# Performance work log

Hardware: AMD Instinct MI355X
Metric: run time of the kernel (lower is better)

The kernel has to match this reference:

```python
import jax, jax.numpy as jnp
import numpy as np

B, S, E, H = 2, 2048, 1024, 16
D = E // H  # head dimension = 64


def setup_inputs() -> dict:
    key = jax.random.key(0)
    ks = jax.random.split(key, 12)
    scale_in = 1.0 / np.sqrt(E)
    x = jax.random.normal(ks[0], (B, S, E), dtype=jnp.float32)
    # random 0/1 attention mask (1 = attend, 0 = masked out)
    mask = jax.random.randint(ks[1], (B, S, S), 0, 2, dtype=jnp.int32)
    # per-head QKV projections, stacked over the head axis: [H, E, D]
    Wq = jax.random.normal(ks[2], (H, E, D), dtype=jnp.float32) * scale_in
    bq = jnp.zeros((H, D), dtype=jnp.float32)
    Wk = jax.random.normal(ks[3], (H, E, D), dtype=jnp.float32) * scale_in
    bk = jnp.zeros((H, D), dtype=jnp.float32)
    Wv = jax.random.normal(ks[4], (H, E, D), dtype=jnp.float32) * scale_in
    bv = jnp.zeros((H, D), dtype=jnp.float32)
    # output projection: [H*D, E] == [E, E]
    Wo = jax.random.normal(ks[5], (H * D, E), dtype=jnp.float32) * scale_in
    bo = jnp.zeros((E,), dtype=jnp.float32)
    return {"x": x, "mask": mask, "Wq": Wq, "bq": bq, "Wk": Wk, "bk": bk,
            "Wv": Wv, "bv": bv, "Wo": Wo, "bo": bo}


def reference(x, mask, Wq, bq, Wk, bk, Wv, bv, Wo, bo):
    # Batched equivalent of the per-head Python loop: all heads at once.
    q = jnp.einsum('bse,hed->bhsd', x, Wq) + bq[None, :, None, :]  # [B,H,S,D]
    k = jnp.einsum('bse,hed->bhsd', x, Wk) + bk[None, :, None, :]
    v = jnp.einsum('bse,hed->bhsd', x, Wv) + bv[None, :, None, :]
    scale = 1.0 / jnp.sqrt(jnp.asarray(D, dtype=q.dtype))
    scores = jnp.einsum('bhsd,bhtd->bhst', q, k) * scale          # [B,H,S,S]
    scores = jnp.where(mask[:, None, :, :] != 0, scores, jnp.asarray(-1e9, scores.dtype))
    attn = jax.nn.softmax(scores, axis=-1)
    ctx = jnp.einsum('bhst,bhtd->bhsd', attn, v)                  # [B,H,S,D]
    # concat heads along feature dim (torch.cat(dim=2))
    concat = jnp.transpose(ctx, (0, 2, 1, 3)).reshape(B, S, H * D)
    return concat @ Wo + bo
```

## Files before the change

### kernel.cpp

```cpp
#include <hip/hip_runtime.h>

#define S_LEN 2048
#define EMB   1024
#define NH    16
#define HD    64
#define BS    2
#define QSCALE 0.18033688f

typedef __bf16 bf16;
typedef bf16  bf16x8 __attribute__((ext_vector_type(8)));
typedef bf16  bf16x4 __attribute__((ext_vector_type(4)));
typedef float f32x4  __attribute__((ext_vector_type(4)));
typedef unsigned long long u64;
typedef unsigned int u32;

__device__ __forceinline__ bf16x8 ld8(const bf16* p){ return *(const bf16x8*)p; }

__device__ __forceinline__ void gl_lds16(const bf16* g, void* l) {
    __builtin_amdgcn_global_load_lds(
        (const __attribute__((address_space(1))) void*)g,
        (__attribute__((address_space(3))) void*)l,
        16, 0, 0);
}

#define SW(row, g) ((((g) ^ ((row) & 7))) * 8)

__global__ __launch_bounds__(256)
void pack_mask(const int* __restrict__ mask, u64* __restrict__ pm)
{
    int lane = threadIdx.x & 63;
    int row  = blockIdx.x * 4 + (threadIdx.x >> 6);
    const int* mr = mask + (size_t)row * S_LEN;
    u64* pr = pm + (size_t)row * (S_LEN / 64);
    for (int i = 0; i < S_LEN / 64; ++i) {
        u64 bits = __ballot(mr[i * 64 + lane] != 0);
        if (lane == 0) pr[i] = bits;
    }
}

__global__ __launch_bounds__(256)
void transpose_w(const float* __restrict__ W0, const float* __restrict__ W1,
                 const float* __restrict__ W2, const float* __restrict__ W3,
                 bf16* __restrict__ Wt)
{
    const int z = blockIdx.z;
    const float* W = z == 0 ? W0 : z == 1 ? W1 : z == 2 ? W2 : W3;
    const bool head = z < 3;
    const int k0 = blockIdx.x * 64, n0 = blockIdx.y * 64;
    const int tid = threadIdx.x;
    __shared__ float T[64][68];
    {
        int k = k0 + (tid >> 2), cg = (tid & 3) * 16;
        size_t base = head ? ((size_t)(n0 >> 6) * ((size_t)EMB * HD) + (size_t)k * HD + cg)
                           : ((size_t)k * EMB + n0 + cg);
        #pragma unroll
        for (int g = 0; g < 4; ++g) {
            f32x4 v = *(const f32x4*)(W + base + g * 4);
            #pragma unroll
            for (int j = 0; j < 4; ++j) T[tid >> 2][cg + g * 4 + j] = v[j];
        }
    }
    __syncthreads();
    {
        int n = n0 + (tid >> 2), ck = (tid & 3) * 16;
        bf16 t16[16];
        #pragma unroll
        for (int j = 0; j < 16; ++j) t16[j] = (bf16)T[ck + j][tid >> 2];
        bf16* outp = Wt + (size_t)z * EMB * EMB + (size_t)n * EMB + k0 + ck;
        *(bf16x8*)outp       = *(bf16x8*)t16;
        *(bf16x8*)(outp + 8) = *(bf16x8*)(t16 + 8);
    }
}

__global__ __launch_bounds__(256)
void cvt_f32_bf16(const float* __restrict__ x, bf16* __restrict__ y)
{
    size_t i = ((size_t)blockIdx.x * 256 + threadIdx.x) * 16;
    bf16 t[16];
    #pragma unroll
    for (int g = 0; g < 4; ++g) {
        f32x4 v = *(const f32x4*)(x + i + g * 4);
        #pragma unroll
        for (int j = 0; j < 4; ++j) t[g * 4 + j] = (bf16)v[j];
    }
    *(bf16x8*)(y + i)     = *(bf16x8*)t;
    *(bf16x8*)(y + i + 8) = *(bf16x8*)(t + 8);
}

__global__ __launch_bounds__(256)
void scale_q(bf16* __restrict__ q)
{
    size_t i = ((size_t)blockIdx.x * 256 + threadIdx.x) * 8;
    bf16x8 v = *(bf16x8*)(q + i);
    #pragma unroll
    for (int j = 0; j < 8; ++j) v[j] = (bf16)((float)v[j] * QSCALE);
    *(bf16x8*)(q + i) = v;
}

__global__ __launch_bounds__(256)
void gemm_qkv(const void* __restrict__ Ap, const bf16* __restrict__ Wt,
              const float* __restrict__ bqp, const float* __restrict__ bkp,
              const float* __restrict__ bvp,
              bf16* __restrict__ qb, bf16* __restrict__ kb, bf16* __restrict__ VT,
              int a32)
{
    const int tid  = threadIdx.x;
    const int lane = tid & 63, quad = lane >> 4, c = lane & 15;
    const int w = tid >> 6, wm = w >> 1, wn = w & 1;
    const int m0 = blockIdx.x * 128;
    const int n0 = blockIdx.y * 128;

    __shared__ bf16 Ash[128][64];
    __shared__ bf16 Wsh[128][64];

    f32x4 acc[4][4];
    #pragma unroll
    for (int mt = 0; mt < 4; ++mt)
        #pragma unroll
        for (int nt = 0; nt < 4; ++nt) acc[mt][nt] = (f32x4){0.f,0.f,0.f,0.f};

    const int lrow = lane >> 3, lcol = (lane & 7) * 8;

    for (int k0 = 0; k0 < EMB; k0 += 64) {
        __syncthreads();
        if (!a32) {
            const bf16* A = (const bf16*)Ap;
            #pragma unroll
            for (int j = 0; j < 4; ++j)
                gl_lds16(A + (size_t)(m0 + w * 32 + j * 8 + lrow) * EMB + k0 + lcol,
                         &Ash[w * 32 + j * 8][0]);
        } else {
            const float* A = (const float*)Ap + (size_t)(m0 + (tid >> 1)) * EMB + k0 + (tid & 1) * 32;
            bf16 t[32];
            #pragma unroll
            for (int g = 0; g < 8; ++g) {
                f32x4 v = *(const f32x4*)(A + g * 4);
                #pragma unroll
                for (int j = 0; j < 4; ++j) t[g * 4 + j] = (bf16)v[j];
            }
            #pragma unroll
            for (int g2 = 0; g2 < 4; ++g2)
                *(bf16x8*)&Ash[tid >> 1][(tid & 1) * 32 + g2 * 8] = *(bf16x8*)(t + g2 * 8);
        }
        #pragma unroll
        for (int j = 0; j < 4; ++j)
            gl_lds16(Wt + (size_t)(n0 + w * 32 + j * 8 + lrow) * EMB + k0 + lcol,
                     &Wsh[w * 32 + j * 8][0]);
        __syncthreads();

        #pragma unroll
        for (int kh = 0; kh < 2; ++kh) {
            bf16x8 af[4], bfv[4];
            #pragma unroll
            for (int mt = 0; mt < 4; ++mt) af[mt]  = ld8(&Ash[wm * 64 + mt * 16 + c][kh * 32 + quad * 8]);
            #pragma unroll
            for (int nt = 0; nt < 4; ++nt) bfv[nt] = ld8(&Wsh[wn * 64 + nt * 16 + c][kh * 32 + quad * 8]);
            #pragma unroll
            for (int mt = 0; mt < 4; ++mt)
                #pragma unroll
                for (int nt = 0; nt < 4; ++nt)
                    acc[mt][nt] = __builtin_amdgcn_mfma_f32_16x16x32_bf16(af[mt], bfv[nt], acc[mt][nt], 0, 0, 0);
        }
    }

    const int z = n0 >> 10;
    const float* bias = z == 0 ? bqp : z == 1 ? bkp : bvp;
    #pragma unroll
    for (int nt = 0; nt < 4; ++nt) {
        int nn = (n0 & 1023) + wn * 64 + nt * 16 + c;
        float bv_ = bias[nn];
        #pragma unroll
        for (int mt = 0; mt < 4; ++mt)
            #pragma unroll
            for (int r = 0; r < 4; ++r) {
                int m = m0 + wm * 64 + mt * 16 + quad * 4 + r;
                float v = acc[mt][nt][r] + bv_;
                if (z == 0)      qb[(size_t)m * EMB + nn] = (bf16)(v * QSCALE);
                else if (z == 1) kb[(size_t)m * EMB + nn] = (bf16)v;
                else {
                    int head = nn >> 6, d = nn & 63;
                    VT[((size_t)((m >> 11) * NH + head) * HD + d) * S_LEN + (m & 2047)] = (bf16)v;
                }
            }
    }
}

__global__ __launch_bounds__(256)
void gemm_o(const bf16* __restrict__ Ap, const bf16* __restrict__ Wt,
            const float* __restrict__ bo, float* __restrict__ C)
{
    const int tid  = threadIdx.x;
    const int lane = tid & 63, quad = lane >> 4, c = lane & 15;
    const int w = tid >> 6, wm = w >> 1, wn = w & 1;
    const int m0 = blockIdx.x * 128;
    const int n0 = blockIdx.y * 64;

    __shared__ bf16 Ash[128][64];
    __shared__ bf16 Wsh[64][64];

    f32x4 acc[4][2];
    #pragma unroll
    for (int mt = 0; mt < 4; ++mt)
        #pragma unroll
        for (int nt = 0; nt < 2; ++nt) acc[mt][nt] = (f32x4){0.f,0.f,0.f,0.f};

    const int lrow = lane >> 3, lcol = (lane & 7) * 8;

    for (int k0 = 0; k0 < EMB; k0 += 64) {
        __syncthreads();
        #pragma unroll
        for (int j = 0; j < 4; ++j)
            gl_lds16(Ap + (size_t)(m0 + w * 32 + j * 8 + lrow) * EMB + k0 + lcol,
                     &Ash[w * 32 + j * 8][0]);
        #pragma unroll
        for (int j = 0; j < 2; ++j)
            gl_lds16(Wt + (size_t)(n0 + w * 16 + j * 8 + lrow) * EMB + k0 + lcol,
                     &Wsh[w * 16 + j * 8][0]);
        __syncthreads();

        #pragma unroll
        for (int kh = 0; kh < 2; ++kh) {
            bf16x8 af[4], bfv[2];
            #pragma unroll
            for (int mt = 0; mt < 4; ++mt) af[mt]  = ld8(&Ash[wm * 64 + mt * 16 + c][kh * 32 + quad * 8]);
            #pragma unroll
            for (int nt = 0; nt < 2; ++nt) bfv[nt] = ld8(&Wsh[wn * 32 + nt * 16 + c][kh * 32 + quad * 8]);
            #pragma unroll
            for (int mt = 0; mt < 4; ++mt)
                #pragma unroll
                for (int nt = 0; nt < 2; ++nt)
                    acc[mt][nt] = __builtin_amdgcn_mfma_f32_16x16x32_bf16(af[mt], bfv[nt], acc[mt][nt], 0, 0, 0);
        }
    }

    #pragma unroll
    for (int nt = 0; nt < 2; ++nt) {
        int n = n0 + wn * 32 + nt * 16 + c;
        float bv_ = bo[n];
        #pragma unroll
        for (int mt = 0; mt < 4; ++mt)
            #pragma unroll
            for (int r = 0; r < 4; ++r) {
                int m = m0 + wm * 64 + mt * 16 + quad * 4 + r;
                C[(size_t)m * EMB + n] = acc[mt][nt][r] + bv_;
            }
    }
}

__global__ __launch_bounds__(512)
void gemm128(const void* __restrict__ Ap, const float* __restrict__ Wp,
             const bf16* __restrict__ Wtp, const float* __restrict__ bias,
             void* __restrict__ Cp, int N, int K, int whead,
             int m_base, int a32, int cmode)
{
    const int tid  = threadIdx.x;
    const int lane = tid & 63, quad = lane >> 4, c = lane & 15;
    const int w = tid >> 6, wm = w >> 2, wn = w & 3;
    const int m0 = blockIdx.x * 128, n0 = blockIdx.y * 128;

    __shared__ bf16 Ash[128][64];
    __shared__ bf16 Wsh[128][64];

    f32x4 acc[4][2];
    #pragma unroll
    for (int mt = 0; mt < 4; ++mt)
        #pragma unroll
        for (int nt = 0; nt < 2; ++nt) acc[mt][nt] = (f32x4){0.f,0.f,0.f,0.f};

    const int arow = tid >> 2, aq = tid & 3;

    auto compute = [&]() {
        #pragma unroll
        for (int kh = 0; kh < 2; ++kh) {
            bf16x8 bfr[2];
            #pragma unroll
            for (int nt = 0; nt < 2; ++nt) {
                int rw = wn * 32 + nt * 16 + c;
                bfr[nt] = ld8(&Wsh[rw][SW(rw, kh * 4 + quad)]);
            }
            #pragma unroll
            for (int mt = 0; mt < 4; ++mt) {
                int ra = wm * 64 + mt * 16 + c;
                bf16x8 af = ld8(&Ash[ra][SW(ra, kh * 4 + quad)]);
                #pragma unroll
                for (int nt = 0; nt < 2; ++nt)
                    acc[mt][nt] = __builtin_amdgcn_mfma_f32_16x16x32_bf16(af, bfr[nt], acc[mt][nt], 0, 0, 0);
            }
        }
    };

    for (int k0 = 0; k0 < K; k0 += 64) {
        __syncthreads();
        if (a32) {
            const float* A = (const float*)Ap + (size_t)(m_base + m0 + arow) * K + k0 + aq * 16;
            bf16 t16[16];
            #pragma unroll
            for (int g = 0; g < 4; ++g) {
                f32x4 v = *(const f32x4*)(A + g * 4);
                #pragma unroll
                for (int j = 0; j < 4; ++j) t16[g * 4 + j] = (bf16)v[j];
            }
            *(bf16x8*)&Ash[arow][SW(arow, aq * 2)]     = *(bf16x8*)t16;
            *(bf16x8*)&Ash[arow][SW(arow, aq * 2 + 1)] = *(bf16x8*)(t16 + 8);
        } else {
            const bf16* A = (const bf16*)Ap + (size_t)(m_base + m0 + arow) * K + k0 + aq * 16;
            *(bf16x8*)&Ash[arow][SW(arow, aq * 2)]     = ld8(A);
            *(bf16x8*)&Ash[arow][SW(arow, aq * 2 + 1)] = ld8(A + 8);
        }
        {
            int nl = tid & 127, kg = tid >> 7;
            int n = n0 + nl;
            size_t base    = whead ? ((size_t)(n >> 6) * ((size_t)K * HD) + (n & 63))
                                   : (size_t)n;
            size_t kstride = whead ? (size_t)HD : (size_t)N;
            #pragma unroll
            for (int p = 0; p < 2; ++p) {
                int grp = kg + 4 * p;
                bf16 t8[8];
                #pragma unroll
                for (int j = 0; j < 8; ++j)
                    t8[j] = (bf16)Wp[base + (size_t)(k0 + grp * 8 + j) * kstride];
                *(bf16x8*)&Wsh[nl][SW(nl, grp)] = *(bf16x8*)t8;
            }
        }
        __syncthreads();
        compute();
    }

    #pragma unroll
    for (int nt = 0; nt < 2; ++nt) {
        int n = n0 + wn * 32 + nt * 16 + c;
        float bv_ = bias[n];
        #pragma unroll
        for (int mt = 0; mt < 4; ++mt)
            #pragma unroll
            for (int r = 0; r < 4; ++r) {
                int m = m0 + wm * 64 + mt * 16 + quad * 4 + r;
                float v = acc[mt][nt][r] + bv_;
                if (cmode == 0)      ((bf16*)Cp)[(size_t)m * N + n] = (bf16)v;
                else if (cmode == 1) ((float*)Cp)[(size_t)m * N + n] = v;
                else {
                    int mm = m_base + m;
                    ((bf16*)Cp)[((size_t)((mm >> 11) * NH + (n >> 6)) * HD + (n & 63)) * S_LEN + (mm & 2047)] = (bf16)v;
                }
            }
    }
}

__global__ __launch_bounds__(256)
void attn_kernel(bf16* q0p, bf16* q1p, const bf16* __restrict__ kbuf,
                 const bf16* __restrict__ VTg, const u64* __restrict__ pmask)
{
    const int tid  = threadIdx.x;
    const int w    = tid >> 6;
    const int lane = tid & 63;
    const int quad = lane >> 4;
    const int c    = lane & 15;
    const int q0   = blockIdx.x * 128;
    const int bh   = blockIdx.y;
    const int b    = bh >> 4, h = bh & 15;

    bf16* qc = b ? q1p : q0p;
    const bf16* kh_ = kbuf + (size_t)b * S_LEN * EMB + h * HD;
    const bf16* vt  = VTg + (size_t)bh * HD * S_LEN;

    __shared__ bf16 Ksh [64][64];
    __shared__ bf16 VTsh[64][64];
    __shared__ bf16 Psh[4][32][64];

    bf16x8 qf[2][2];
    #pragma unroll
    for (int st = 0; st < 2; ++st)
        #pragma unroll
        for (int kk = 0; kk < 2; ++kk)
            qf[st][kk] = ld8(qc + (size_t)(q0 + w * 32 + st * 16 + c) * EMB + h * HD + kk * 32 + quad * 8);

    const u64* pmr0 = pmask + (size_t)(b * S_LEN + q0 + w * 32 + c) * (S_LEN / 64);
    const u64* pmr1 = pmr0 + (size_t)16 * (S_LEN / 64);

    f32x4 l4[2] = {(f32x4){0.f,0.f,0.f,0.f}, (f32x4){0.f,0.f,0.f,0.f}};
    f32x4 o[2][4];
    #pragma unroll
    for (int st = 0; st < 2; ++st)
        #pragma unroll
        for (int dt = 0; dt < 4; ++dt) o[st][dt] = (f32x4){0.f,0.f,0.f,0.f};

    const int srow = tid >> 2, sg = (tid & 3) * 2;
    bf16x8 kr[2], vr[2];
    auto loadKV = [&](int t0) {
        const bf16* kp = kh_ + (size_t)(t0 + srow) * EMB + sg * 8;
        kr[0] = ld8(kp); kr[1] = ld8(kp + 8);
        const bf16* vp = vt + (size_t)srow * S_LEN + t0 + sg * 8;
        vr[0] = ld8(vp); vr[1] = ld8(vp + 8);
    };

    loadKV(0);
    for (int t0 = 0; t0 < S_LEN; t0 += 64) {
        __syncthreads();
        #pragma unroll
        for (int g2 = 0; g2 < 2; ++g2) {
            *(bf16x8*)&Ksh [srow][SW(srow, sg + g2)] = kr[g2];
            *(bf16x8*)&VTsh[srow][SW(srow, sg + g2)] = vr[g2];
        }
        __syncthreads();
        if (t0 + 64 < S_LEN) loadKV(t0 + 64);

        u64 s0 = pmr0[t0 >> 6] >> (quad * 4);
        u64 s1 = pmr1[t0 >> 6] >> (quad * 4);
        u32 mm[2][2] = {{(u32)s0, (u32)(s0 >> 32)}, {(u32)s1, (u32)(s1 >> 32)}};

        f32x4 sc[2][4];
        #pragma unroll
        for (int st = 0; st < 2; ++st)
            #pragma unroll
            for (int tt = 0; tt < 4; ++tt) sc[st][tt] = (f32x4){0.f,0.f,0.f,0.f};
        #pragma unroll
        for (int tt = 0; tt < 4; ++tt)
            #pragma unroll
            for (int kk = 0; kk < 2; ++kk) {
                int rk = tt * 16 + c;
                bf16x8 ka = ld8(&Ksh[rk][SW(rk, kk * 4 + quad)]);
                sc[0][tt] = __builtin_amdgcn_mfma_f32_16x16x32_bf16(ka, qf[0][kk], sc[0][tt], 0, 0, 0);
                sc[1][tt] = __builtin_amdgcn_mfma_f32_16x16x32_bf16(ka, qf[1][kk], sc[1][tt], 0, 0, 0);
            }

        #pragma unroll
        for (int st = 0; st < 2; ++st) {
            int prow = st * 16 + c;
            #pragma unroll
            for (int tt = 0; tt < 4; ++tt) {
                u32 half = mm[st][tt >> 1];
                bf16x4 pv;
                #pragma unroll
                for (int r = 0; r < 4; ++r) {
                    float e = __builtin_amdgcn_exp2f(sc[st][tt][r]);
                    e = ((half >> ((tt & 1) * 16 + r)) & 1) ? e : 0.f;
                    l4[st][r] += e;
                    pv[r] = (bf16)e;
                }
                *(bf16x4*)&Psh[w][prow][SW(prow, tt * 2 + (quad >> 1)) + (quad & 1) * 4] = pv;
            }
        }
        __builtin_amdgcn_s_waitcnt(0xc07f);

        #pragma unroll
        for (int th = 0; th < 2; ++th) {
            bf16x8 pf0 = ld8(&Psh[w][c]     [SW(c,      th * 4 + quad)]);
            bf16x8 pf1 = ld8(&Psh[w][16 + c][SW(16 + c, th * 4 + quad)]);
            #pragma unroll
            for (int dt = 0; dt < 4; ++dt) {
                int rv = dt * 16 + c;
                bf16x8 av = ld8(&VTsh[rv][SW(rv, th * 4 + quad)]);
                o[0][dt] = __builtin_amdgcn_mfma_f32_16x16x32_bf16(av, pf0, o[0][dt], 0, 0, 0);
                o[1][dt] = __builtin_amdgcn_mfma_f32_16x16x32_bf16(av, pf1, o[1][dt], 0, 0, 0);
            }
        }
    }

    #pragma unroll
    for (int st = 0; st < 2; ++st) {
        float ls = l4[st][0] + l4[st][1] + l4[st][2] + l4[st][3];
        ls += __shfl_xor(ls, 16);
        ls += __shfl_xor(ls, 32);
        float inv = 1.0f / fmaxf(ls, 1e-30f);
        #pragma unroll
        for (int dt = 0; dt < 4; ++dt) {
            bf16x4 ov;
            #pragma unroll
            for (int r = 0; r < 4; ++r) ov[r] = (bf16)(o[st][dt][r] * inv);
            *(bf16x4*)&qc[(size_t)(q0 + w * 32 + st * 16 + c) * EMB + h * HD + dt * 16 + quad * 4] = ov;
        }
    }
}

extern "C" void kernel_launch(void* const* d_in, const int* in_sizes, int n_in,
                              void* d_out, int out_size, void* d_ws, size_t ws_size,
                              hipStream_t stream)
{
    const float* x    = (const float*)d_in[0];
    const int*   mask = (const int*)d_in[1];
    const float* Wq   = (const float*)d_in[2];
    const float* bq   = (const float*)d_in[3];
    const float* Wk   = (const float*)d_in[4];
    const float* bk   = (const float*)d_in[5];
    const float* Wv   = (const float*)d_in[6];
    const float* bv   = (const float*)d_in[7];
    const float* Wo   = (const float*)d_in[8];
    const float* bo   = (const float*)d_in[9];
    float* out = (float*)d_out;

    const size_t SLAB = (size_t)S_LEN * EMB;
    const size_t QB = (size_t)BS * SLAB * sizeof(bf16);
    const size_t WT = (size_t)4 * EMB * EMB * sizeof(bf16);
    const size_t PM = (size_t)BS * S_LEN * (S_LEN / 64) * 8;
    const size_t XB = (size_t)BS * SLAB * sizeof(bf16);

    bf16* VT = (bf16*)d_out;
    bf16* kb = (bf16*)d_out + BS * SLAB;

    dim3 b256(256), b512(512);
    dim3 gAtt (S_LEN / 128, BS * NH);
    dim3 gT   (EMB / 64, EMB / 64, 4);
    dim3 gPk  (BS * S_LEN / 4);
    dim3 gFull(BS * S_LEN / 128, EMB / 128);
    dim3 gHalf(S_LEN / 128, EMB / 128);

    if (ws_size >= QB + WT + PM + 64) {
        bf16* qb  = (bf16*)d_ws;
        bf16* Wt  = (bf16*)((char*)d_ws + QB);
        u64*  pm  = (u64*)((char*)d_ws + QB + WT);
        const void* xA = x; int a32 = 1;
        if (ws_size >= QB + WT + PM + XB + 64) {
            bf16* xbf = (bf16*)((char*)d_ws + QB + WT + PM);
            cvt_f32_bf16<<<dim3(1024), b256, 0, stream>>>(x, xbf);
            xA = xbf; a32 = 0;
        }
        pack_mask<<<gPk, b256, 0, stream>>>(mask, pm);
        transpose_w<<<gT, b256, 0, stream>>>(Wq, Wk, Wv, Wo, Wt);

        gemm_qkv<<<dim3(BS * S_LEN / 128, 3 * EMB / 128), b256, 0, stream>>>(
            xA, Wt, bq, bk, bv, qb, kb, VT, a32);

        attn_kernel<<<gAtt, b256, 0, stream>>>(qb, qb + SLAB, kb, VT, pm);

        gemm_o<<<dim3(BS * S_LEN / 128, EMB / 64), b256, 0, stream>>>(
            qb, Wt + (size_t)3 * EMB * EMB, bo, out);
    } else if (ws_size >= QB + PM + 64) {
        bf16* qb = (bf16*)d_ws;
        u64*  pm = (u64*)((char*)d_ws + QB);
        pack_mask<<<gPk, b256, 0, stream>>>(mask, pm);

        gemm128<<<gFull, b512, 0, stream>>>(x, Wk, nullptr, bk, kb, EMB, EMB, 1, 0, 1, 0);
        gemm128<<<gFull, b512, 0, stream>>>(x, Wv, nullptr, bv, VT, EMB, EMB, 1, 0, 1, 2);
        gemm128<<<gFull, b512, 0, stream>>>(x, Wq, nullptr, bq, qb, EMB, EMB, 1, 0, 1, 0);
        scale_q<<<dim3(BS * SLAB / (256 * 8)), b256, 0, stream>>>(qb);

        attn_kernel<<<gAtt, b256, 0, stream>>>(qb, qb + SLAB, kb, VT, pm);

        gemm128<<<gFull, b512, 0, stream>>>(qb, Wo, nullptr, bo, out, EMB, EMB, 0, 0, 0, 1);
    } else {
        bf16* qb0 = (bf16*)d_in[4];
        bf16* qb1 = (bf16*)d_in[6];
        u64*  pm  = (u64*)d_in[2];

        gemm128<<<gFull, b512, 0, stream>>>(x, Wk, nullptr, bk, kb, EMB, EMB, 1, 0, 1, 0);
        gemm128<<<gFull, b512, 0, stream>>>(x, Wv, nullptr, bv, VT, EMB, EMB, 1, 0, 1, 2);
        gemm128<<<gHalf, b512, 0, stream>>>(x, Wq, nullptr, bq, qb0, EMB, EMB, 1, 0,     1, 0);
        gemm128<<<gHalf, b512, 0, stream>>>(x, Wq, nullptr, bq, qb1, EMB, EMB, 1, S_LEN, 1, 0);
        scale_q<<<dim3(SLAB / (256 * 8)), b256, 0, stream>>>(qb0);
        scale_q<<<dim3(SLAB / (256 * 8)), b256, 0, stream>>>(qb1);
        pack_mask<<<gPk, b256, 0, stream>>>(mask, pm);

        attn_kernel<<<gAtt, b256, 0, stream>>>(qb0, qb1, kb, VT, pm);

        gemm128<<<gHalf, b512, 0, stream>>>(qb0, Wo, nullptr, bo, out,        EMB, EMB, 0, 0, 0, 1);
        gemm128<<<gHalf, b512, 0, stream>>>(qb1, Wo, nullptr, bo, out + SLAB, EMB, EMB, 0, 0, 0, 1);
    }
}
```

Baseline: 260.4 us.

## Use 512-thread attention blocks with double-buffered K/V LDS tiles

The attention kernel now runs 8 waves per 128-query block, each owning 16 query rows instead of 32. K and V^T tiles are double-buffered in LDS, which drops one __syncthreads per iteration, and each thread loads half as many K/V elements. Launch-bounds occupancy hints are added to the QKV and output GEMMs. The trade-off is more LDS per block and fewer MFMAs per wave between barriers. The single remaining barrier per step relies on the double buffer to avoid overwriting data still being read.

```diff
diff --git a/kernel.cpp b/kernel.cpp
--- a/kernel.cpp
+++ b/kernel.cpp
@@ -97,7 +97,7 @@
     *(bf16x8*)(q + i) = v;
 }
 
-__global__ __launch_bounds__(256)
+__global__ __launch_bounds__(256, 3)
 void gemm_qkv(const void* __restrict__ Ap, const bf16* __restrict__ Wt,
               const float* __restrict__ bqp, const float* __restrict__ bkp,
               const float* __restrict__ bvp,
@@ -185,7 +185,7 @@
     }
 }
 
-__global__ __launch_bounds__(256)
+__global__ __launch_bounds__(256, 4)
 void gemm_o(const bf16* __restrict__ Ap, const bf16* __restrict__ Wt,
             const float* __restrict__ bo, float* __restrict__ C)
 {
@@ -347,7 +347,7 @@
     }
 }
 
-__global__ __launch_bounds__(256)
+__global__ __launch_bounds__(512, 2)
 void attn_kernel(bf16* q0p, bf16* q1p, const bf16* __restrict__ kbuf,
                  const bf16* __restrict__ VTg, const u64* __restrict__ pmask)
 {
@@ -364,112 +364,90 @@
     const bf16* kh_ = kbuf + (size_t)b * S_LEN * EMB + h * HD;
     const bf16* vt  = VTg + (size_t)bh * HD * S_LEN;
 
-    __shared__ bf16 Ksh [64][64];
-    __shared__ bf16 VTsh[64][64];
-    __shared__ bf16 Psh[4][32][64];
-
-    bf16x8 qf[2][2];
-    #pragma unroll
-    for (int st = 0; st < 2; ++st)
-        #pragma unroll
-        for (int kk = 0; kk < 2; ++kk)
-            qf[st][kk] = ld8(qc + (size_t)(q0 + w * 32 + st * 16 + c) * EMB + h * HD + kk * 32 + quad * 8);
-
-    const u64* pmr0 = pmask + (size_t)(b * S_LEN + q0 + w * 32 + c) * (S_LEN / 64);
-    const u64* pmr1 = pmr0 + (size_t)16 * (S_LEN / 64);
-
-    f32x4 l4[2] = {(f32x4){0.f,0.f,0.f,0.f}, (f32x4){0.f,0.f,0.f,0.f}};
-    f32x4 o[2][4];
-    #pragma unroll
-    for (int st = 0; st < 2; ++st)
-        #pragma unroll
-        for (int dt = 0; dt < 4; ++dt) o[st][dt] = (f32x4){0.f,0.f,0.f,0.f};
-
-    const int srow = tid >> 2, sg = (tid & 3) * 2;
-    bf16x8 kr[2], vr[2];
+    __shared__ bf16 Ksh [2][64][64];
+    __shared__ bf16 VTsh[2][64][64];
+    __shared__ bf16 Psh[8][16][64];
+
+    bf16x8 qf[2];
+    #pragma unroll
+    for (int kk = 0; kk < 2; ++kk)
+        qf[kk] = ld8(qc + (size_t)(q0 + w * 16 + c) * EMB + h * HD + kk * 32 + quad * 8);
+
+    const u64* pmr = pmask + (size_t)(b * S_LEN + q0 + w * 16 + c) * (S_LEN / 64);
+
+    f32x4 l4 = (f32x4){0.f,0.f,0.f,0.f};
+    f32x4 o[4];
+    #pragma unroll
+    for (int dt = 0; dt < 4; ++dt) o[dt] = (f32x4){0.f,0.f,0.f,0.f};
+
+    const int srow = tid >> 3, sg = tid & 7;
+    bf16x8 kr, vr;
     auto loadKV = [&](int t0) {
-        const bf16* kp = kh_ + (size_t)(t0 + srow) * EMB + sg * 8;
-        kr[0] = ld8(kp); kr[1] = ld8(kp + 8);
-        const bf16* vp = vt + (size_t)srow * S_LEN + t0 + sg * 8;
-        vr[0] = ld8(vp); vr[1] = ld8(vp + 8);
+        kr = ld8(kh_ + (size_t)(t0 + srow) * EMB + sg * 8);
+        vr = ld8(vt + (size_t)srow * S_LEN + t0 + sg * 8);
     };
 
     loadKV(0);
+    int buf = 0;
     for (int t0 = 0; t0 < S_LEN; t0 += 64) {
-        __syncthreads();
-        #pragma unroll
-        for (int g2 = 0; g2 < 2; ++g2) {
-            *(bf16x8*)&Ksh [srow][SW(srow, sg + g2)] = kr[g2];
-            *(bf16x8*)&VTsh[srow][SW(srow, sg + g2)] = vr[g2];
-        }
+        *(bf16x8*)&Ksh [buf][srow][SW(srow, sg)] = kr;
+        *(bf16x8*)&VTsh[buf][srow][SW(srow, sg)] = vr;
         __syncthreads();
         if (t0 + 64 < S_LEN) loadKV(t0 + 64);
 
-        u64 s0 = pmr0[t0 >> 6] >> (quad * 4);
-        u64 s1 = pmr1[t0 >> 6] >> (quad * 4);
-        u32 mm[2][2] = {{(u32)s0, (u32)(s0 >> 32)}, {(u32)s1, (u32)(s1 >> 32)}};
-
-        f32x4 sc[2][4];
-        #pragma unroll
-        for (int st = 0; st < 2; ++st)
-            #pragma unroll
-            for (int tt = 0; tt < 4; ++tt) sc[st][tt] = (f32x4){0.f,0.f,0.f,0.f};
+        u64 s0 = pmr[t0 >> 6] >> (quad * 4);
+        u32 mm[2] = {(u32)s0, (u32)(s0 >> 32)};
+
+        f32x4 sc[4];
+        #pragma unroll
+        for (int tt = 0; tt < 4; ++tt) sc[tt] = (f32x4){0.f,0.f,0.f,0.f};
         #pragma unroll
         for (int tt = 0; tt < 4; ++tt)
             #pragma unroll
             for (int kk = 0; kk < 2; ++kk) {
                 int rk = tt * 16 + c;
-                bf16x8 ka = ld8(&Ksh[rk][SW(rk, kk * 4 + quad)]);
-                sc[0][tt] = __builtin_amdgcn_mfma_f32_16x16x32_bf16(ka, qf[0][kk], sc[0][tt], 0, 0, 0);
-                sc[1][tt] = __builtin_amdgcn_mfma_f32_16x16x32_bf16(ka, qf[1][kk], sc[1][tt], 0, 0, 0);
-            }
-
-        #pragma unroll
-        for (int st = 0; st < 2; ++st) {
-            int prow = st * 16 + c;
-            #pragma unroll
-            for (int tt = 0; tt < 4; ++tt) {
-                u32 half = mm[st][tt >> 1];
-                bf16x4 pv;
-                #pragma unroll
-                for (int r = 0; r < 4; ++r) {
-                    float e = __builtin_amdgcn_exp2f(sc[st][tt][r]);
-                    e = ((half >> ((tt & 1) * 16 + r)) & 1) ? e : 0.f;
-                    l4[st][r] += e;
-                    pv[r] = (bf16)e;
-                }
-                *(bf16x4*)&Psh[w][prow][SW(prow, tt * 2 + (quad >> 1)) + (quad & 1) * 4] = pv;
-            }
+                bf16x8 ka = ld8(&Ksh[buf][rk][SW(rk, kk * 4 + quad)]);
+                sc[tt] = __builtin_amdgcn_mfma_f32_16x16x32_bf16(ka, qf[kk], sc[tt], 0, 0, 0);
+            }
+
+        #pragma unroll
+        for (int tt = 0; tt < 4; ++tt) {
+            u32 half = mm[tt >> 1];
+            bf16x4 pv;
+            #pragma unroll
+            for (int r = 0; r < 4; ++r) {
+                float e = __builtin_amdgcn_exp2f(sc[tt][r]);
+                e = ((half >> ((tt & 1) * 16 + r)) & 1) ? e : 0.f;
+                l4[r] += e;
+                pv[r] = (bf16)e;
+            }
+            *(bf16x4*)&Psh[w][c][SW(c, tt * 2 + (quad >> 1)) + (quad & 1) * 4] = pv;
         }
         __builtin_amdgcn_s_waitcnt(0xc07f);
 
         #pragma unroll
         for (int th = 0; th < 2; ++th) {
-            bf16x8 pf0 = ld8(&Psh[w][c]     [SW(c,      th * 4 + quad)]);
-            bf16x8 pf1 = ld8(&Psh[w][16 + c][SW(16 + c, th * 4 + quad)]);
+            bf16x8 pf = ld8(&Psh[w][c][SW(c, th * 4 + quad)]);
             #pragma unroll
             for (int dt = 0; dt < 4; ++dt) {
                 int rv = dt * 16 + c;
-                bf16x8 av = ld8(&VTsh[rv][SW(rv, th * 4 + quad)]);
-                o[0][dt] = __builtin_amdgcn_mfma_f32_16x16x32_bf16(av, pf0, o[0][dt], 0, 0, 0);
-                o[1][dt] = __builtin_amdgcn_mfma_f32_16x16x32_bf16(av, pf1, o[1][dt], 0, 0, 0);
-            }
-        }
-    }
-
-    #pragma unroll
-    for (int st = 0; st < 2; ++st) {
-        float ls = l4[st][0] + l4[st][1] + l4[st][2] + l4[st][3];
-        ls += __shfl_xor(ls, 16);
-        ls += __shfl_xor(ls, 32);
-        float inv = 1.0f / fmaxf(ls, 1e-30f);
-        #pragma unroll
-        for (int dt = 0; dt < 4; ++dt) {
-            bf16x4 ov;
-            #pragma unroll
-            for (int r = 0; r < 4; ++r) ov[r] = (bf16)(o[st][dt][r] * inv);
-            *(bf16x4*)&qc[(size_t)(q0 + w * 32 + st * 16 + c) * EMB + h * HD + dt * 16 + quad * 4] = ov;
-        }
+                bf16x8 av = ld8(&VTsh[buf][rv][SW(rv, th * 4 + quad)]);
+                o[dt] = __builtin_amdgcn_mfma_f32_16x16x32_bf16(av, pf, o[dt], 0, 0, 0);
+            }
+        }
+        buf ^= 1;
+    }
+
+    float ls = l4[0] + l4[1] + l4[2] + l4[3];
+    ls += __shfl_xor(ls, 16);
+    ls += __shfl_xor(ls, 32);
+    float inv = 1.0f / fmaxf(ls, 1e-30f);
+    #pragma unroll
+    for (int dt = 0; dt < 4; ++dt) {
+        bf16x4 ov;
+        #pragma unroll
+        for (int r = 0; r < 4; ++r) ov[r] = (bf16)(o[dt][r] * inv);
+        *(bf16x4*)&qc[(size_t)(q0 + w * 16 + c) * EMB + h * HD + dt * 16 + quad * 4] = ov;
     }
 }
 
@@ -521,7 +499,7 @@
         gemm_qkv<<<dim3(BS * S_LEN / 128, 3 * EMB / 128), b256, 0, stream>>>(
             xA, Wt, bq, bk, bv, qb, kb, VT, a32);
 
-        attn_kernel<<<gAtt, b256, 0, stream>>>(qb, qb + SLAB, kb, VT, pm);
+        attn_kernel<<<gAtt, b512, 0, stream>>>(qb, qb + SLAB, kb, VT, pm);
 
         gemm_o<<<dim3(BS * S_LEN / 128, EMB / 64), b256, 0, stream>>>(
             qb, Wt + (size_t)3 * EMB * EMB, bo, out);
@@ -535,7 +513,7 @@
         gemm128<<<gFull, b512, 0, stream>>>(x, Wq, nullptr, bq, qb, EMB, EMB, 1, 0, 1, 0);
         scale_q<<<dim3(BS * SLAB / (256 * 8)), b256, 0, stream>>>(qb);
 
-        attn_kernel<<<gAtt, b256, 0, stream>>>(qb, qb + SLAB, kb, VT, pm);
+        attn_kernel<<<gAtt, b512, 0, stream>>>(qb, qb + SLAB, kb, VT, pm);
 
         gemm128<<<gFull, b512, 0, stream>>>(qb, Wo, nullptr, bo, out, EMB, EMB, 0, 0, 0, 1);
     } else {
@@ -551,7 +529,7 @@
         scale_q<<<dim3(SLAB / (256 * 8)), b256, 0, stream>>>(qb1);
         pack_mask<<<gPk, b256, 0, stream>>>(mask, pm);
 
-        attn_kernel<<<gAtt, b256, 0, stream>>>(qb0, qb1, kb, VT, pm);
+        attn_kernel<<<gAtt, b512, 0, stream>>>(qb0, qb1, kb, VT, pm);
 
         gemm128<<<gHalf, b512, 0, stream>>>(qb0, Wo, nullptr, bo, out,        EMB, EMB, 0, 0, 0, 1);
         gemm128<<<gHalf, b512, 0, stream>>>(qb1, Wo, nullptr, bo, out + SLAB, EMB, EMB, 0, 0, 0, 1);
```

Result: faster. 244.2 us (-6.2%).
